# Kernel tuning notes

Measured on AMD Instinct MI355X. Metric: run time of the kernel, lower is better.

Reference implementation:

```python
import jax, jax.numpy as jnp
import numpy as np

N_NODES = 100000
N_EDGES = 1600000
IN_DIM = 128
HID_DIM = 128


def setup_inputs() -> dict:
    key = jax.random.key(0)
    k_x, k_e, k_w1, k_w2, k_b1, k_b2 = jax.random.split(key, 6)
    x = jax.random.normal(k_x, (N_NODES, IN_DIM), dtype=jnp.float32)
    edge_index = jax.random.randint(k_e, (2, N_EDGES), 0, N_NODES, dtype=jnp.int64)
    # GCNConv params: linear weight (no bias in lin), plus post-aggregation bias
    s1 = 1.0 / np.sqrt(IN_DIM)
    s2 = 1.0 / np.sqrt(HID_DIM)
    W1 = jax.random.uniform(k_w1, (IN_DIM, HID_DIM), jnp.float32, -s1, s1)
    b1 = jnp.zeros((HID_DIM,), jnp.float32)
    W2 = jax.random.uniform(k_w2, (HID_DIM, HID_DIM), jnp.float32, -s2, s2)
    b2 = jnp.zeros((HID_DIM,), jnp.float32)
    return {"x": x, "edge_index": edge_index, "W1": W1, "b1": b1, "W2": W2, "b2": b2}


def _gcn_conv(x, row, col, norm, W, b, n_nodes):
    # h = x W ; out[col] += norm * h[row] ; + b   (PyG GCNConv math)
    h = x @ W
    msg = h[row] * norm[:, None]          # [E+N, H] edge-gathered messages
    out = jax.ops.segment_sum(msg, col, num_segments=n_nodes)
    return out + b


def reference(x, edge_index, W1, b1, W2, b2):
    n = x.shape[0]
    # add self-loops (PyG gcn_norm default: add_self_loops=True, edge_weight=1)
    loop = jnp.arange(n, dtype=edge_index.dtype)
    row = jnp.concatenate([edge_index[0], loop])
    col = jnp.concatenate([edge_index[1], loop])
    # symmetric normalization: deg computed at col (target)
    deg = jax.ops.segment_sum(jnp.ones(row.shape[0], x.dtype), col, num_segments=n)
    dis = jnp.where(deg > 0, jax.lax.rsqrt(jnp.maximum(deg, 1e-30)), 0.0)
    norm = dis[row] * dis[col]            # [E+N]
    h = _gcn_conv(x, row, col, norm, W1, b1, n)
    h = jax.nn.relu(h)
    out = _gcn_conv(h, row, col, norm, W2, b2, n)
    return out
```

## Files before the change

kernel.cpp:

```cpp
#include <hip/hip_runtime.h>

#define NN 100000
#define NE 1600000
#define FD 128
#define NBUK 196
#define BCAP 9216
#define EPBB 8192
#define NBB 196
#define NGROUP 6250
#define GEMM_BLKS 1563

typedef unsigned int  u32;
typedef unsigned short u16;
typedef __bf16 bf16x8 __attribute__((ext_vector_type(8)));
typedef float  f32x4v __attribute__((ext_vector_type(4)));

__device__ __forceinline__ u16 f2bf(float f) {
    u32 u = __float_as_uint(f);
    u32 r = (u + 0x7FFFu + ((u >> 16) & 1u)) >> 16;
    return (u16)r;
}

__device__ __forceinline__ void acc2(float& x, float& y, float wt, u32 w) {
    x += wt * __uint_as_float(w << 16);
    y += wt * __uint_as_float(w & 0xffff0000u);
}
__device__ __forceinline__ void acc8(float4& L, float4& H, float wt, uint4 u) {
    acc2(L.x, L.y, wt, u.x); acc2(L.z, L.w, wt, u.y);
    acc2(H.x, H.y, wt, u.z); acc2(H.z, H.w, wt, u.w);
}

__global__ void k_init_pack(int* __restrict__ bcur,
                            const float* __restrict__ W1, const float* __restrict__ W2,
                            u16* __restrict__ Wf1, u16* __restrict__ Wf2) {
    if (blockIdx.x == 0) {
        if (threadIdx.x < NBUK) bcur[threadIdx.x] = threadIdx.x * BCAP;
        return;
    }
    int tid = (blockIdx.x - 1) * 256 + threadIdx.x;
    if (tid >= 2048) return;
    int l = tid & 63;
    int tq = tid >> 6;
    int q = tq & 3, t = tq >> 2;
    int n = t * 16 + (l & 15);
    int k0 = q * 32 + (l >> 4) * 8;
    u32 p[4], r[4];
    for (int jj = 0; jj < 4; ++jj) {
        u16 lo1 = f2bf(W1[(size_t)(k0 + 2 * jj) * FD + n]);
        u16 hi1 = f2bf(W1[(size_t)(k0 + 2 * jj + 1) * FD + n]);
        p[jj] = (u32)lo1 | ((u32)hi1 << 16);
        u16 lo2 = f2bf(W2[(size_t)(k0 + 2 * jj) * FD + n]);
        u16 hi2 = f2bf(W2[(size_t)(k0 + 2 * jj + 1) * FD + n]);
        r[jj] = (u32)lo2 | ((u32)hi2 << 16);
    }
    *(uint4*)&Wf1[(size_t)tid * 8] = make_uint4(p[0], p[1], p[2], p[3]);
    *(uint4*)&Wf2[(size_t)tid * 8] = make_uint4(r[0], r[1], r[2], r[3]);
}

__global__ __launch_bounds__(256, 4) void k_mega(const int* __restrict__ row,
                                                 const int* __restrict__ col,
                                                 int* __restrict__ bcur,
                                                 u32* __restrict__ ebuf,
                                                 const float* __restrict__ x,
                                                 const u16* __restrict__ Wf1,
                                                 u16* __restrict__ hb) {
    __shared__ u16 smem[16384];
    const int tid = threadIdx.x;

    if (blockIdx.x < NBB) {
        int* hist = (int*)smem;
        for (int i = tid; i < NBUK; i += 256) hist[i] = 0;
        __syncthreads();
        const int e0 = blockIdx.x * EPBB;
        const int e1 = min(e0 + EPBB, NE);
        for (int e = e0 + tid; e < e1; e += 256)
            atomicAdd(&hist[col[e] >> 9], 1);
        __syncthreads();
        for (int i = tid; i < NBUK; i += 256) {
            int c = hist[i];
            hist[i] = c ? atomicAdd(&bcur[i], c) : 0;
        }
        __syncthreads();
        for (int e = e0 + tid; e < e1; e += 256) {
            int c = col[e];
            int pos = atomicAdd(&hist[c >> 9], 1);
            ebuf[pos] = ((u32)row[e] << 9) | (u32)(c & 511);
        }
        return;
    }

    {
        const uint4* s = (const uint4*)Wf1;
        uint4* d = (uint4*)smem;
#pragma unroll
        for (int i = 0; i < 8; ++i) d[tid + 256 * i] = s[tid + 256 * i];
    }
    __syncthreads();

    const int wave = tid >> 6, lane = tid & 63;
    const int gid = (blockIdx.x - NBB) * 4 + wave;
    if (gid >= NGROUP) return;
    const int row0 = gid * 16;
    const int lr = lane & 15;
    const int lh = lane >> 4;

    f32x4v acc[8];
#pragma unroll
    for (int t = 0; t < 8; ++t) { f32x4v z = {0.f, 0.f, 0.f, 0.f}; acc[t] = z; }

#pragma unroll
    for (int q = 0; q < 4; ++q) {
        const float* arow = x + (size_t)(row0 + lr) * FD + lh * 8 + q * 32;
        float4 f0 = *(const float4*)(arow);
        float4 f1 = *(const float4*)(arow + 4);
        union { bf16x8 v; u16 s[8]; } ua;
        ua.s[0] = f2bf(f0.x); ua.s[1] = f2bf(f0.y);
        ua.s[2] = f2bf(f0.z); ua.s[3] = f2bf(f0.w);
        ua.s[4] = f2bf(f1.x); ua.s[5] = f2bf(f1.y);
        ua.s[6] = f2bf(f1.z); ua.s[7] = f2bf(f1.w);
        bf16x8 a = ua.v;
#pragma unroll
        for (int t = 0; t < 8; ++t) {
            bf16x8 bfr = *(const bf16x8*)(&smem[(size_t)(t * 4 + q) * 512 + lane * 8]);
            acc[t] = __builtin_amdgcn_mfma_f32_16x16x32_bf16(a, bfr, acc[t], 0, 0, 0);
        }
    }
#pragma unroll
    for (int t = 0; t < 8; ++t) {
#pragma unroll
        for (int j = 0; j < 4; ++j) {
            const int r = row0 + lh * 4 + j;
            hb[(size_t)r * FD + t * 16 + lr] = f2bf(acc[t][j]);
        }
    }
}

__global__ __launch_bounds__(256) void k_bucket(const u32* __restrict__ ebuf,
                                                const int* __restrict__ bcur,
                                                int* __restrict__ nstart,
                                                int* __restrict__ ndeg,
                                                float* __restrict__ dis,
                                                int* __restrict__ srcs) {
    __shared__ int lcnt[512];
    __shared__ int s[256];
    const int tid = threadIdx.x;
    const int b = blockIdx.x;
    const int base = b * BCAP;
    const int end = bcur[b];

    lcnt[tid] = 0; lcnt[tid + 256] = 0;
    __syncthreads();
    for (int i = base + tid; i < end; i += 256)
        atomicAdd(&lcnt[ebuf[i] & 511], 1);
    __syncthreads();

    const int c0 = lcnt[tid * 2], c1 = lcnt[tid * 2 + 1];
    s[tid] = c0 + c1;
    __syncthreads();
    for (int off = 1; off < 256; off <<= 1) {
        int t = 0;
        if (tid >= off) t = s[tid - off];
        __syncthreads();
        if (tid >= off) s[tid] += t;
        __syncthreads();
    }
    const int excl = (tid == 0) ? 0 : s[tid - 1];
    __syncthreads();
    lcnt[tid * 2] = excl;
    lcnt[tid * 2 + 1] = excl + c0;

    const int v0 = b * 512 + tid * 2;
    if (v0 < NN) {
        nstart[v0] = base + excl;
        ndeg[v0] = c0;
        dis[v0] = rsqrtf((float)c0 + 1.0f);
    }
    if (v0 + 1 < NN) {
        nstart[v0 + 1] = base + excl + c0;
        ndeg[v0 + 1] = c1;
        dis[v0 + 1] = rsqrtf((float)c1 + 1.0f);
    }
    __syncthreads();

    for (int i = base + tid; i < end; i += 256) {
        u32 p = ebuf[i];
        int pos = atomicAdd(&lcnt[p & 511], 1);
        srcs[base + pos] = (int)(p >> 9);
    }
}

__global__ __launch_bounds__(256) void k_agg2(const u16* __restrict__ hb,
                                              const float* __restrict__ b1,
                                              const float* __restrict__ dis,
                                              const int* __restrict__ nstart,
                                              const int* __restrict__ ndeg,
                                              const int* __restrict__ srcs,
                                              const u16* __restrict__ Wf2,
                                              u16* __restrict__ hb2) {
    __shared__ u16 tile[16 * 136];
    const int tid = threadIdx.x;
    const int nl = tid >> 4;
    const int f8 = tid & 15;
    const int v = blockIdx.x * 16 + nl;
    const uint4* h4 = (const uint4*)hb;

    const float dv = dis[v];
    float4 aL = ((const float4*)b1)[f8 * 2];
    float4 aH = ((const float4*)b1)[f8 * 2 + 1];
    {
        const float sl = dv * dv;
        uint4 u = h4[(size_t)v * 16 + f8];
        acc8(aL, aH, sl, u);
    }

    int e = nstart[v];
    const int end = e + ndeg[v];
    for (; e + 3 < end; e += 4) {
        const int s0 = srcs[e], s1 = srcs[e + 1], s2 = srcs[e + 2], s3 = srcs[e + 3];
        const float w0 = dv * dis[s0];
        const float w1 = dv * dis[s1];
        const float w2 = dv * dis[s2];
        const float w3 = dv * dis[s3];
        const uint4 u0 = h4[(size_t)s0 * 16 + f8];
        const uint4 u1 = h4[(size_t)s1 * 16 + f8];
        const uint4 u2 = h4[(size_t)s2 * 16 + f8];
        const uint4 u3 = h4[(size_t)s3 * 16 + f8];
        acc8(aL, aH, w0, u0); acc8(aL, aH, w1, u1);
        acc8(aL, aH, w2, u2); acc8(aL, aH, w3, u3);
    }
    for (; e < end; ++e) {
        const int s0 = srcs[e];
        const float w0 = dv * dis[s0];
        const uint4 u0 = h4[(size_t)s0 * 16 + f8];
        acc8(aL, aH, w0, u0);
    }

    {
        uint4 p;
        p.x = (u32)f2bf(fmaxf(aL.x, 0.f)) | ((u32)f2bf(fmaxf(aL.y, 0.f)) << 16);
        p.y = (u32)f2bf(fmaxf(aL.z, 0.f)) | ((u32)f2bf(fmaxf(aL.w, 0.f)) << 16);
        p.z = (u32)f2bf(fmaxf(aH.x, 0.f)) | ((u32)f2bf(fmaxf(aH.y, 0.f)) << 16);
        p.w = (u32)f2bf(fmaxf(aH.z, 0.f)) | ((u32)f2bf(fmaxf(aH.w, 0.f)) << 16);
        *(uint4*)&tile[nl * 136 + f8 * 8] = p;
    }
    __syncthreads();

    const int wave = tid >> 6, lane = tid & 63;
    const int lr = lane & 15;
    const int lh = lane >> 4;
    f32x4v a0 = {0.f, 0.f, 0.f, 0.f}, a1 = {0.f, 0.f, 0.f, 0.f};
#pragma unroll
    for (int q = 0; q < 4; ++q) {
        bf16x8 a = *(const bf16x8*)&tile[lr * 136 + q * 32 + lh * 8];
        bf16x8 bb0 = *(const bf16x8*)&Wf2[(size_t)((2 * wave) * 4 + q) * 512 + lane * 8];
        bf16x8 bb1 = *(const bf16x8*)&Wf2[(size_t)((2 * wave + 1) * 4 + q) * 512 + lane * 8];
        a0 = __builtin_amdgcn_mfma_f32_16x16x32_bf16(a, bb0, a0, 0, 0, 0);
        a1 = __builtin_amdgcn_mfma_f32_16x16x32_bf16(a, bb1, a1, 0, 0, 0);
    }
    const int row0 = blockIdx.x * 16;
#pragma unroll
    for (int j = 0; j < 4; ++j) {
        const int r = row0 + lh * 4 + j;
        hb2[(size_t)r * FD + (2 * wave) * 16 + lr] = f2bf(a0[j]);
        hb2[(size_t)r * FD + (2 * wave + 1) * 16 + lr] = f2bf(a1[j]);
    }
}

__global__ __launch_bounds__(256) void k_agg_f32(const u16* __restrict__ hb,
                                                 const float* __restrict__ b,
                                                 const float* __restrict__ dis,
                                                 const int* __restrict__ nstart,
                                                 const int* __restrict__ ndeg,
                                                 const int* __restrict__ srcs,
                                                 float* __restrict__ out) {
    const int v = (blockIdx.x * 256 + threadIdx.x) >> 4;
    if (v >= NN) return;
    const int f8 = threadIdx.x & 15;
    const uint4* h4 = (const uint4*)hb;

    const float dv = dis[v];
    float4 aL = ((const float4*)b)[f8 * 2];
    float4 aH = ((const float4*)b)[f8 * 2 + 1];
    {
        const float sl = dv * dv;
        uint4 u = h4[(size_t)v * 16 + f8];
        acc8(aL, aH, sl, u);
    }

    int e = nstart[v];
    const int end = e + ndeg[v];
    for (; e + 3 < end; e += 4) {
        const int s0 = srcs[e], s1 = srcs[e + 1], s2 = srcs[e + 2], s3 = srcs[e + 3];
        const float w0 = dv * dis[s0];
        const float w1 = dv * dis[s1];
        const float w2 = dv * dis[s2];
        const float w3 = dv * dis[s3];
        const uint4 u0 = h4[(size_t)s0 * 16 + f8];
        const uint4 u1 = h4[(size_t)s1 * 16 + f8];
        const uint4 u2 = h4[(size_t)s2 * 16 + f8];
        const uint4 u3 = h4[(size_t)s3 * 16 + f8];
        acc8(aL, aH, w0, u0); acc8(aL, aH, w1, u1);
        acc8(aL, aH, w2, u2); acc8(aL, aH, w3, u3);
    }
    for (; e < end; ++e) {
        const int s0 = srcs[e];
        const float w0 = dv * dis[s0];
        const uint4 u0 = h4[(size_t)s0 * 16 + f8];
        acc8(aL, aH, w0, u0);
    }

    float4* o = (float4*)out;
    o[(size_t)v * 32 + f8 * 2] = aL;
    o[(size_t)v * 32 + f8 * 2 + 1] = aH;
}


extern "C" void kernel_launch(void* const* d_in, const int* in_sizes, int n_in,
                              void* d_out, int out_size, void* d_ws, size_t ws_size,
                              hipStream_t stream) {
    const float* x  = (const float*)d_in[0];
    const int*   ei = (const int*)d_in[1];
    const float* W1 = (const float*)d_in[2];
    const float* b1 = (const float*)d_in[3];
    const float* W2 = (const float*)d_in[4];
    const float* b2 = (const float*)d_in[5];
    float* out = (float*)d_out;

    const int* row = ei;
    const int* col = ei + NE;

    char* base = (char*)d_ws;
    size_t o = 0;
    auto take = [&](size_t bytes) -> void* {
        void* p = base + o;
        o += (bytes + 255) & ~(size_t)255;
        return p;
    };
    int*   nstart  = (int*)take((size_t)NN * 4);
    int*   ndeg    = (int*)take((size_t)NN * 4);
    int*   bcur    = (int*)take(256 * 4);
    float* dis     = (float*)take((size_t)NN * 4);
    u16*   Wf1     = (u16*)take(16384 * 2);
    u16*   Wf2     = (u16*)take(16384 * 2);
    u16*   hb      = (u16*)take((size_t)NN * FD * 2);
    u16*   hb2     = (u16*)take((size_t)NN * FD * 2);
    int*   srcs    = (int*)take((size_t)NBUK * BCAP * 4);
    u32*   ebuf    = (u32*)take((size_t)NBUK * BCAP * 4);

    k_init_pack<<<9, 256, 0, stream>>>(bcur, W1, W2, Wf1, Wf2);
    k_mega<<<NBB + GEMM_BLKS, 256, 0, stream>>>(row, col, bcur, ebuf, x, Wf1, hb);
    k_bucket<<<NBUK, 256, 0, stream>>>(ebuf, bcur, nstart, ndeg, dis, srcs);
    k_agg2<<<NGROUP, 256, 0, stream>>>(hb, b1, dis, nstart, ndeg, srcs, Wf2, hb2);
    k_agg_f32<<<NGROUP, 256, 0, stream>>>(hb2, b2, dis, nstart, ndeg, srcs, out);
}
```

Baseline: 198.6 us.

## Split edge binning out and overlap per-bucket CSR build with first GEMM

Moves edge binning into its own kernel with twice as many smaller blocks, then fuses the per-bucket counting, prefix scan and source scatter with the X·W1 MFMA GEMM in a single launch so the two run concurrently. Previously binning overlapped the GEMM and bucketing ran alone afterwards. The final output store also becomes a nontemporal store to avoid polluting cache. The cost is a different overlap pairing. The bucket blocks read ebuf, which is scattered randomly and more irregular than the sequential binning reads.

```diff
diff --git a/kernel.cpp b/kernel.cpp
--- a/kernel.cpp
+++ b/kernel.cpp
@@ -5,8 +5,8 @@
 #define FD 128
 #define NBUK 196
 #define BCAP 9216
-#define EPBB 8192
-#define NBB 196
+#define EPBB 4096
+#define NBB 391
 #define NGROUP 6250
 #define GEMM_BLKS 1563
 
@@ -57,48 +57,102 @@
     *(uint4*)&Wf2[(size_t)tid * 8] = make_uint4(r[0], r[1], r[2], r[3]);
 }
 
-__global__ __launch_bounds__(256, 4) void k_mega(const int* __restrict__ row,
-                                                 const int* __restrict__ col,
-                                                 int* __restrict__ bcur,
-                                                 u32* __restrict__ ebuf,
-                                                 const float* __restrict__ x,
-                                                 const u16* __restrict__ Wf1,
-                                                 u16* __restrict__ hb) {
+__global__ __launch_bounds__(256) void k_bin(const int* __restrict__ row,
+                                             const int* __restrict__ col,
+                                             int* __restrict__ bcur,
+                                             u32* __restrict__ ebuf) {
+    __shared__ int hist[NBUK];
+    const int tid = threadIdx.x;
+    for (int i = tid; i < NBUK; i += 256) hist[i] = 0;
+    __syncthreads();
+    const int e0 = blockIdx.x * EPBB;
+    const int e1 = min(e0 + EPBB, NE);
+    for (int e = e0 + tid; e < e1; e += 256)
+        atomicAdd(&hist[col[e] >> 9], 1);
+    __syncthreads();
+    for (int i = tid; i < NBUK; i += 256) {
+        int c = hist[i];
+        hist[i] = c ? atomicAdd(&bcur[i], c) : 0;
+    }
+    __syncthreads();
+    for (int e = e0 + tid; e < e1; e += 256) {
+        int c = col[e];
+        int pos = atomicAdd(&hist[c >> 9], 1);
+        ebuf[pos] = ((u32)row[e] << 9) | (u32)(c & 511);
+    }
+}
+
+__global__ __launch_bounds__(256, 4) void k_mega2(const u32* __restrict__ ebuf,
+                                                  const int* __restrict__ bcur,
+                                                  int* __restrict__ nstart,
+                                                  int* __restrict__ ndeg,
+                                                  float* __restrict__ dis,
+                                                  int* __restrict__ srcs,
+                                                  const float* __restrict__ x,
+                                                  const u16* __restrict__ Wf1,
+                                                  u16* __restrict__ hb) {
     __shared__ u16 smem[16384];
     const int tid = threadIdx.x;
 
-    if (blockIdx.x < NBB) {
-        int* hist = (int*)smem;
-        for (int i = tid; i < NBUK; i += 256) hist[i] = 0;
-        __syncthreads();
-        const int e0 = blockIdx.x * EPBB;
-        const int e1 = min(e0 + EPBB, NE);
-        for (int e = e0 + tid; e < e1; e += 256)
-            atomicAdd(&hist[col[e] >> 9], 1);
-        __syncthreads();
-        for (int i = tid; i < NBUK; i += 256) {
-            int c = hist[i];
-            hist[i] = c ? atomicAdd(&bcur[i], c) : 0;
-        }
-        __syncthreads();
-        for (int e = e0 + tid; e < e1; e += 256) {
-            int c = col[e];
-            int pos = atomicAdd(&hist[c >> 9], 1);
-            ebuf[pos] = ((u32)row[e] << 9) | (u32)(c & 511);
+    if (blockIdx.x < NBUK) {
+        int* lcnt = (int*)smem;
+        int* s = lcnt + 512;
+        const int b = blockIdx.x;
+        const int base = b * BCAP;
+        const int end = bcur[b];
+
+        lcnt[tid] = 0; lcnt[tid + 256] = 0;
+        __syncthreads();
+        for (int i = base + tid; i < end; i += 256)
+            atomicAdd(&lcnt[ebuf[i] & 511], 1);
+        __syncthreads();
+
+        const int c0 = lcnt[tid * 2], c1 = lcnt[tid * 2 + 1];
+        s[tid] = c0 + c1;
+        __syncthreads();
+        for (int off = 1; off < 256; off <<= 1) {
+            int t = 0;
+            if (tid >= off) t = s[tid - off];
+            __syncthreads();
+            if (tid >= off) s[tid] += t;
+            __syncthreads();
+        }
+        const int excl = (tid == 0) ? 0 : s[tid - 1];
+        __syncthreads();
+        lcnt[tid * 2] = excl;
+        lcnt[tid * 2 + 1] = excl + c0;
+
+        const int v0 = b * 512 + tid * 2;
+        if (v0 < NN) {
+            nstart[v0] = base + excl;
+            ndeg[v0] = c0;
+            dis[v0] = rsqrtf((float)c0 + 1.0f);
+        }
+        if (v0 + 1 < NN) {
+            nstart[v0 + 1] = base + excl + c0;
+            ndeg[v0 + 1] = c1;
+            dis[v0 + 1] = rsqrtf((float)c1 + 1.0f);
+        }
+        __syncthreads();
+
+        for (int i = base + tid; i < end; i += 256) {
+            u32 p = ebuf[i];
+            int pos = atomicAdd(&lcnt[p & 511], 1);
+            srcs[base + pos] = (int)(p >> 9);
         }
         return;
     }
 
     {
-        const uint4* s = (const uint4*)Wf1;
+        const uint4* s4 = (const uint4*)Wf1;
         uint4* d = (uint4*)smem;
 #pragma unroll
-        for (int i = 0; i < 8; ++i) d[tid + 256 * i] = s[tid + 256 * i];
+        for (int i = 0; i < 8; ++i) d[tid + 256 * i] = s4[tid + 256 * i];
     }
     __syncthreads();
 
     const int wave = tid >> 6, lane = tid & 63;
-    const int gid = (blockIdx.x - NBB) * 4 + wave;
+    const int gid = (blockIdx.x - NBUK) * 4 + wave;
     if (gid >= NGROUP) return;
     const int row0 = gid * 16;
     const int lr = lane & 15;
@@ -132,60 +186,6 @@
             const int r = row0 + lh * 4 + j;
             hb[(size_t)r * FD + t * 16 + lr] = f2bf(acc[t][j]);
         }
-    }
-}
-
-__global__ __launch_bounds__(256) void k_bucket(const u32* __restrict__ ebuf,
-                                                const int* __restrict__ bcur,
-                                                int* __restrict__ nstart,
-                                                int* __restrict__ ndeg,
-                                                float* __restrict__ dis,
-                                                int* __restrict__ srcs) {
-    __shared__ int lcnt[512];
-    __shared__ int s[256];
-    const int tid = threadIdx.x;
-    const int b = blockIdx.x;
-    const int base = b * BCAP;
-    const int end = bcur[b];
-
-    lcnt[tid] = 0; lcnt[tid + 256] = 0;
-    __syncthreads();
-    for (int i = base + tid; i < end; i += 256)
-        atomicAdd(&lcnt[ebuf[i] & 511], 1);
-    __syncthreads();
-
-    const int c0 = lcnt[tid * 2], c1 = lcnt[tid * 2 + 1];
-    s[tid] = c0 + c1;
-    __syncthreads();
-    for (int off = 1; off < 256; off <<= 1) {
-        int t = 0;
-        if (tid >= off) t = s[tid - off];
-        __syncthreads();
-        if (tid >= off) s[tid] += t;
-        __syncthreads();
-    }
-    const int excl = (tid == 0) ? 0 : s[tid - 1];
-    __syncthreads();
-    lcnt[tid * 2] = excl;
-    lcnt[tid * 2 + 1] = excl + c0;
-
-    const int v0 = b * 512 + tid * 2;
-    if (v0 < NN) {
-        nstart[v0] = base + excl;
-        ndeg[v0] = c0;
-        dis[v0] = rsqrtf((float)c0 + 1.0f);
-    }
-    if (v0 + 1 < NN) {
-        nstart[v0 + 1] = base + excl + c0;
-        ndeg[v0 + 1] = c1;
-        dis[v0 + 1] = rsqrtf((float)c1 + 1.0f);
-    }
-    __syncthreads();
-
-    for (int i = base + tid; i < end; i += 256) {
-        u32 p = ebuf[i];
-        int pos = atomicAdd(&lcnt[p & 511], 1);
-        srcs[base + pos] = (int)(p >> 9);
     }
 }
 
@@ -309,9 +309,11 @@
         acc8(aL, aH, w0, u0);
     }
 
-    float4* o = (float4*)out;
-    o[(size_t)v * 32 + f8 * 2] = aL;
-    o[(size_t)v * 32 + f8 * 2 + 1] = aH;
+    f32x4v vL = {aL.x, aL.y, aL.z, aL.w};
+    f32x4v vH = {aH.x, aH.y, aH.z, aH.w};
+    f32x4v* o = (f32x4v*)out;
+    __builtin_nontemporal_store(vL, &o[(size_t)v * 32 + f8 * 2]);
+    __builtin_nontemporal_store(vH, &o[(size_t)v * 32 + f8 * 2 + 1]);
 }
 
 
@@ -348,8 +350,9 @@
     u32*   ebuf    = (u32*)take((size_t)NBUK * BCAP * 4);
 
     k_init_pack<<<9, 256, 0, stream>>>(bcur, W1, W2, Wf1, Wf2);
-    k_mega<<<NBB + GEMM_BLKS, 256, 0, stream>>>(row, col, bcur, ebuf, x, Wf1, hb);
-    k_bucket<<<NBUK, 256, 0, stream>>>(ebuf, bcur, nstart, ndeg, dis, srcs);
+    k_bin<<<NBB, 256, 0, stream>>>(row, col, bcur, ebuf);
+    k_mega2<<<NBUK + GEMM_BLKS, 256, 0, stream>>>(ebuf, bcur, nstart, ndeg, dis, srcs,
+                                                  x, Wf1, hb);
     k_agg2<<<NGROUP, 256, 0, stream>>>(hb, b1, dis, nstart, ndeg, srcs, Wf2, hb2);
     k_agg_f32<<<NGROUP, 256, 0, stream>>>(hb2, b2, dis, nstart, ndeg, srcs, out);
 }
```

Measured after the change: 192.6 us. 3.0% less time.
